# Optimization experiments

Measured on AMD Instinct MI355X. Metric: run time of the kernel, lower is better.

The kernel has to match this reference:

```python
import jax, jax.numpy as jnp
import numpy as np

jax.config.update("jax_enable_x64", True)

P = 2013265921        # NTT-friendly prime (15 * 2^27 + 1), stand-in for BLS12-381 Fr
G_ROOT = 31           # primitive root of P
LOG_N = 21
N = 1 << LOG_N


def _bit_reverse_perm(n):
    logn = n.bit_length() - 1
    idx = np.arange(n, dtype=np.int64)
    rev = np.zeros(n, dtype=np.int64)
    for b in range(logn):
        rev = (rev << 1) | ((idx >> b) & 1)
    return rev


def _pow_arr(base, exps, mod):
    # vectorized modular exponentiation over numpy int64 exponents (host-side, trace-time)
    res = np.ones_like(exps)
    b = np.int64(base % mod)
    e = exps.copy()
    while e.max() > 0:
        res = np.where(e & 1, (res * b) % mod, res)
        b = (b * b) % mod
        e >>= 1
    return res


_REV = _bit_reverse_perm(N)


def intt(x):
    """Inverse NTT over Z_P, radix-2 DIT with bit-reversal. x: [N] int64 in [0,P)."""
    root = pow(G_ROOT, (P - 1) // N, P)
    iroot = pow(root, P - 2, P)
    x = x[_REV]
    length = 2
    while length <= N:
        half = length // 2
        wlen = pow(iroot, N // length, P)
        tw = jnp.asarray(_pow_arr(wlen, np.arange(half, dtype=np.int64), P))  # [half]
        x = x.reshape(-1, length)
        even, odd = x[:, :half], x[:, half:]
        t = (odd * tw) % P                       # products < 2^62, exact in int64
        x = jnp.concatenate([(even + t) % P, (even - t) % P], axis=1).reshape(-1)
        length *= 2
    n_inv = pow(N, P - 2, P)
    return (x * n_inv) % P


def compress4(a, b, c, d, z):
    """zkp.compress: a + z*b + z^2*c + z^3*d  (mod P). z is a Python int challenge."""
    z1 = z % P
    z2 = (z1 * z1) % P
    z3 = (z2 * z1) % P
    return (a + (b * z1) % P + (c * z2) % P + (d * z3) % P) % P


def commit(poly, bases):
    """KZG commitment proxy: MSM reduced to a scalar-weighted sum of SRS bases."""
    scal = poly.astype(jnp.float32) * np.float32(1.0 / P)  # normalize field elems
    return jnp.einsum('n,nc->c', scal, bases)              # [3]


def reference(w_l, w_r, w_o, w_4, table1, table2, table3, table4,
              q_lookup, powers_of_g, zeta):
    # Round 1: wire polynomials via INTT + commitments via MSM
    w_l_poly = intt(w_l)
    w_r_poly = intt(w_r)
    w_o_poly = intt(w_o)
    w_4_poly = intt(w_4)

    # Lookup: compress tables with zeta, build query table f, split sorted multiset
    t_comp = compress4(table1, table2, table3, table4, zeta)
    table_poly = intt(t_comp)
    w_comp = compress4(w_l, w_r, w_o, w_4, zeta)
    f_comp = jnp.where(q_lookup != 0, w_comp, t_comp)      # compute_query_table
    f_poly = intt(f_comp)

    s = jnp.sort(jnp.concatenate([t_comp, f_comp]))        # combine_split
    h_1, h_2 = s[0::2], s[1::2]
    h_1_poly = intt(h_1)
    h_2_poly = intt(h_2)

    polys = jnp.stack([w_l_poly, w_r_poly, w_o_poly, w_4_poly,
                       table_poly, f_poly, h_1_poly, h_2_poly])  # [8, N]
    commits = jnp.stack([commit(p, powers_of_g) for p in polys])  # [8, 3]
    return commits, polys


def setup_inputs() -> dict:
    key = jax.random.key(0)
    ks = jax.random.split(key, 11)
    fe = lambda k: jax.random.randint(k, (N,), 0, P, dtype=jnp.int64)
    return {
        'w_l': fe(ks[0]), 'w_r': fe(ks[1]), 'w_o': fe(ks[2]), 'w_4': fe(ks[3]),
        'table1': fe(ks[4]), 'table2': fe(ks[5]), 'table3': fe(ks[6]), 'table4': fe(ks[7]),
        'q_lookup': jax.random.randint(ks[8], (N,), 0, 2, dtype=jnp.int64),
        'powers_of_g': jax.random.normal(ks[9], (N, 3), dtype=jnp.float32),
        'zeta': 987654321,
    }
```

## Files before the change

### kernel.cpp

```cpp
#include <hip/hip_runtime.h>
#include <stdint.h>

#define PRIME 2013265921u
#define LOGN 21
#define NN (1u << LOGN)

constexpr uint32_t cpow(uint64_t b, uint64_t e) {
    uint64_t r = 1;
    b %= PRIME;
    while (e) {
        if (e & 1ull) r = r * b % PRIME;
        b = b * b % PRIME;
        e >>= 1;
    }
    return (uint32_t)r;
}
constexpr uint32_t cpinv() {
    uint32_t inv = 1;
    for (int i = 0; i < 6; i++) inv *= 2u - PRIME * inv;
    return inv;
}
constexpr uint32_t NPRIME   = (uint32_t)(0u - cpinv());
constexpr uint32_t RMODP    = (uint32_t)((1ull << 32) % PRIME);
constexpr uint32_t ROOT     = cpow(31u, (PRIME - 1) / NN);
constexpr uint32_t IROOT    = cpow(ROOT, PRIME - 2);
constexpr uint32_t IROOT1K  = cpow(IROOT, 1024);
constexpr uint32_t NINV     = cpow(NN, PRIME - 2);
constexpr uint32_t NINV_M   = (uint32_t)((((uint64_t)NINV) << 32) % PRIME);

__device__ __forceinline__ uint32_t addmod(uint32_t a, uint32_t b) {
    uint32_t s = a + b; return (s >= PRIME) ? s - PRIME : s;
}
__device__ __forceinline__ uint32_t submod(uint32_t a, uint32_t b) {
    return (a >= b) ? (a - b) : (a + PRIME - b);
}
__device__ __forceinline__ uint32_t mulmod(uint32_t a, uint32_t b) {
    return (uint32_t)(((uint64_t)a * (uint64_t)b) % PRIME);
}
__device__ __forceinline__ uint32_t montmul(uint32_t a, uint32_t b) {
    uint64_t t = (uint64_t)a * b;
    uint32_t m = (uint32_t)t * NPRIME;
    uint32_t u = (uint32_t)((t + (uint64_t)m * PRIME) >> 32);
    return (u >= PRIME) ? u - PRIME : u;
}
__device__ uint32_t powmod(uint32_t b, uint32_t e) {
    uint32_t r = 1u;
    while (e) {
        if (e & 1u) r = mulmod(r, b);
        b = mulmod(b, b);
        e >>= 1;
    }
    return r;
}
__device__ __forceinline__ uint32_t tomont(uint32_t x) {
    return (uint32_t)((((uint64_t)x) << 32) % PRIME);
}

__global__ void twiddle_ab_kernel(uint32_t* __restrict__ A, uint32_t* __restrict__ B) {
    uint32_t i = blockIdx.x * blockDim.x + threadIdx.x;
    B[i] = tomont(powmod(IROOT, i));
    A[i] = tomont(powmod(IROOT1K, i));
}
__global__ void twiddle_compact_kernel(const uint32_t* __restrict__ A, const uint32_t* __restrict__ B,
                                       uint32_t* __restrict__ WT1, uint32_t* __restrict__ ROWT,
                                       uint32_t* __restrict__ CW) {
    uint32_t i = blockIdx.x * blockDim.x + threadIdx.x;
    if (i < 4096) {
        if (i == 0) WT1[0] = RMODP;
        else {
            uint32_t s = 31u - __clz(i);
            uint32_t j = i ^ (1u << s);
            uint32_t e = j << (20u - s);
            WT1[i] = montmul(A[e >> 10], B[e & 1023u]);
        }
    }
    if (i < 512) {
        if (i == 0) ROWT[0] = RMODP;
        else {
            uint32_t t = 31u - __clz(i);
            uint32_t e = (i - (1u << t)) << (20u - t);
            ROWT[i] = montmul(A[e >> 10], B[e & 1023u]);
        }
    }
    if (i < 36864) {
        uint32_t s = i >> 12, j = i & 4095u;
        uint32_t e = j << (8u - s);
        CW[i] = montmul(A[e >> 10], B[e & 1023u]);
    }
}

__global__ __launch_bounds__(256) void compress_kernel(
        const int* __restrict__ wl, const int* __restrict__ wr,
        const int* __restrict__ wo, const int* __restrict__ w4,
        const int* __restrict__ t1, const int* __restrict__ t2,
        const int* __restrict__ t3, const int* __restrict__ t4,
        const int* __restrict__ q,  const int* __restrict__ zp,
        uint32_t* __restrict__ tcomp, uint32_t* __restrict__ fcomp,
        unsigned int* __restrict__ hist64) {
    __shared__ unsigned int h64[64];
    if (threadIdx.x < 64) h64[threadIdx.x] = 0;
    __syncthreads();
    uint32_t z1 = ((uint32_t)zp[0]) % PRIME;
    uint32_t z2 = mulmod(z1, z1);
    uint32_t z3 = mulmod(z2, z1);
    for (uint32_t i = blockIdx.x * blockDim.x + threadIdx.x; i < NN; i += gridDim.x * blockDim.x) {
        uint32_t t = addmod(addmod((uint32_t)t1[i], mulmod((uint32_t)t2[i], z1)),
                            addmod(mulmod((uint32_t)t3[i], z2), mulmod((uint32_t)t4[i], z3)));
        uint32_t w = addmod(addmod((uint32_t)wl[i], mulmod((uint32_t)wr[i], z1)),
                            addmod(mulmod((uint32_t)wo[i], z2), mulmod((uint32_t)w4[i], z3)));
        uint32_t f = (q[i] != 0) ? w : t;
        tcomp[i] = t;
        fcomp[i] = f;
        atomicAdd(&h64[t >> 25], 1u);
        atomicAdd(&h64[f >> 25], 1u);
    }
    __syncthreads();
    if (threadIdx.x < 64 && h64[threadIdx.x])
        atomicAdd(&hist64[threadIdx.x], h64[threadIdx.x]);
}

#define NBUCK 8192

__global__ void scan64_kernel(const unsigned int* __restrict__ hist64,
                              unsigned int* __restrict__ cbase, unsigned int* __restrict__ ccursor) {
    if (threadIdx.x == 0) {
        unsigned int run = 0;
        for (int b = 0; b < 64; b++) { cbase[b] = run; ccursor[b] = run; run += hist64[b]; }
        cbase[64] = run;
    }
}

__global__ __launch_bounds__(256) void pass1_kernel(const uint32_t* __restrict__ tcomp,
                                                    const uint32_t* __restrict__ fcomp,
                                                    unsigned int* __restrict__ ccursor,
                                                    uint32_t* __restrict__ barr1) {
    __shared__ uint32_t grp[4096];
    __shared__ unsigned char grpb[4096];
    __shared__ unsigned int cnt[64], pref[64], curs[64], rbase[64];
    uint32_t base = blockIdx.x * 4096;
    uint32_t tid = threadIdx.x;
    if (tid < 64) cnt[tid] = 0;
    __syncthreads();
    for (uint32_t l = tid; l < 4096; l += 256) {
        uint32_t gi = base + l;
        uint32_t v = (gi < NN) ? tcomp[gi] : fcomp[gi - NN];
        atomicAdd(&cnt[v >> 25], 1u);
    }
    __syncthreads();
    if (tid == 0) {
        unsigned int run = 0;
        for (int b = 0; b < 64; b++) { pref[b] = run; curs[b] = run; run += cnt[b]; }
    }
    __syncthreads();
    if (tid < 64 && cnt[tid]) rbase[tid] = atomicAdd(&ccursor[tid], cnt[tid]);
    for (uint32_t l = tid; l < 4096; l += 256) {
        uint32_t gi = base + l;
        uint32_t v = (gi < NN) ? tcomp[gi] : fcomp[gi - NN];
        uint32_t b = v >> 25;
        unsigned int p = atomicAdd(&curs[b], 1u);
        grp[p] = v; grpb[p] = (unsigned char)b;
    }
    __syncthreads();
    for (uint32_t l = tid; l < 4096; l += 256) {
        uint32_t b = grpb[l];
        barr1[rbase[b] + (l - pref[b])] = grp[l];
    }
}

__global__ __launch_bounds__(256) void fine_hist_kernel(const uint32_t* __restrict__ barr1,
                                                        const unsigned int* __restrict__ cbase,
                                                        unsigned int* __restrict__ hist) {
    __shared__ unsigned int cnt[128];
    uint32_t tid = threadIdx.x;
    uint32_t reg = blockIdx.y;
    if (tid < 128) cnt[tid] = 0;
    __syncthreads();
    uint32_t lo = cbase[reg], hi = cbase[reg + 1];
    for (uint32_t i = lo + blockIdx.x * 256 + tid; i < hi; i += gridDim.x * 256)
        atomicAdd(&cnt[(barr1[i] >> 18) & 127u], 1u);
    __syncthreads();
    if (tid < 128 && cnt[tid]) atomicAdd(&hist[reg * 128 + tid], cnt[tid]);
}

__global__ void scan_kernel(const unsigned int* __restrict__ hist,
                            unsigned int* __restrict__ basearr, unsigned int* __restrict__ fcursor) {
    __shared__ unsigned int ls[256];
    int t = threadIdx.x;
    unsigned int local[32];
    unsigned int s = 0;
    for (int k = 0; k < 32; k++) { local[k] = hist[t * 32 + k]; s += local[k]; }
    ls[t] = s;
    __syncthreads();
    for (int off = 1; off < 256; off <<= 1) {
        unsigned int v = (t >= off) ? ls[t - off] : 0u;
        __syncthreads();
        ls[t] += v;
        __syncthreads();
    }
    unsigned int run = ls[t] - s;
    for (int k = 0; k < 32; k++) {
        basearr[t * 32 + k] = run;
        fcursor[t * 32 + k] = run;
        run += local[k];
    }
    if (t == 255) basearr[NBUCK] = run;
}

__global__ __launch_bounds__(256) void pass2_kernel(const uint32_t* __restrict__ barr1,
                                                    const unsigned int* __restrict__ cbase,
                                                    unsigned int* __restrict__ fcursor,
                                                    uint32_t* __restrict__ barr2) {
    __shared__ uint32_t grp[4096];
    __shared__ unsigned char grpb[4096];
    __shared__ unsigned int cnt[128], pref[128], curs[128], rbase[128];
    uint32_t tid = threadIdx.x;
    uint32_t reg = blockIdx.y;
    uint32_t lo = cbase[reg], hi = cbase[reg + 1];
    for (uint32_t start = lo + blockIdx.x * 4096; start < hi; start += gridDim.x * 4096) {
        uint32_t n = min(4096u, hi - start);
        if (tid < 128) cnt[tid] = 0;
        __syncthreads();
        for (uint32_t l = tid; l < n; l += 256)
            atomicAdd(&cnt[(barr1[start + l] >> 18) & 127u], 1u);
        __syncthreads();
        if (tid == 0) {
            unsigned int run = 0;
            for (int b = 0; b < 128; b++) { pref[b] = run; curs[b] = run; run += cnt[b]; }
        }
        __syncthreads();
        if (tid < 128 && cnt[tid]) rbase[tid] = atomicAdd(&fcursor[reg * 128 + tid], cnt[tid]);
        for (uint32_t l = tid; l < n; l += 256) {
            uint32_t v = barr1[start + l];
            uint32_t b = (v >> 18) & 127u;
            unsigned int p = atomicAdd(&curs[b], 1u);
            grp[p] = v; grpb[p] = (unsigned char)b;
        }
        __syncthreads();
        for (uint32_t l = tid; l < n; l += 256) {
            uint32_t b = grpb[l];
            barr2[rbase[b] + (l - pref[b])] = grp[l];
        }
        __syncthreads();
    }
}

__global__ __launch_bounds__(256) void bucket_sort_kernel(const uint32_t* __restrict__ barr,
                                                          const unsigned int* __restrict__ basearr,
                                                          uint32_t* __restrict__ h1, uint32_t* __restrict__ h2) {
    __shared__ uint32_t ord[4096];
    __shared__ unsigned int cnt[128], pref[128], curs[128];
    uint32_t b  = blockIdx.x;
    uint32_t lo = basearr[b], hi = basearr[b + 1];
    uint32_t n  = hi - lo;
    if (n == 0) return;
    if (n > 4096) n = 4096;
    uint32_t tid = threadIdx.x;
    if (tid < 128) cnt[tid] = 0;
    __syncthreads();
    for (uint32_t i = tid; i < n; i += 256)
        atomicAdd(&cnt[(barr[lo + i] >> 11) & 127u], 1u);
    __syncthreads();
    if (tid == 0) {
        unsigned int run = 0;
        for (int d = 0; d < 128; d++) { pref[d] = run; curs[d] = run; run += cnt[d]; }
    }
    __syncthreads();
    for (uint32_t i = tid; i < n; i += 256) {
        uint32_t v = barr[lo + i];
        uint32_t d = (v >> 11) & 127u;
        unsigned int p = atomicAdd(&curs[d], 1u);
        ord[p] = v;
    }
    __syncthreads();
    for (uint32_t p = tid; p < n; p += 256) {
        uint32_t v = ord[p];
        uint32_t d = (v >> 11) & 127u;
        uint32_t l0 = pref[d], l1 = l0 + cnt[d];
        uint32_t r = 0;
        for (uint32_t q = l0; q < l1; q++) {
            uint32_t u = ord[q];
            r += (u < v) || (u == v && q < p);
        }
        uint32_t gp = lo + l0 + r;
        if (gp & 1) h2[gp >> 1] = v; else h1[gp >> 1] = v;
    }
}

struct SrcPtrs { const uint32_t* p[8]; };

__global__ void bitrev_kernel(SrcPtrs srcs, uint32_t* __restrict__ dst) {
    __shared__ uint32_t tile[64 * 65];
    uint32_t poly = blockIdx.y;
    const uint32_t* src = srcs.p[poly];
    uint32_t* out = dst + (size_t)poly * NN;
    uint32_t m  = blockIdx.x;
    uint32_t rm = __brev(m) >> 23;
    for (uint32_t l = threadIdx.x; l < 4096; l += blockDim.x) {
        uint32_t u = l >> 6, v = l & 63;
        tile[u * 65 + v] = src[(u << 15) | (rm << 6) | v];
    }
    __syncthreads();
    for (uint32_t l = threadIdx.x; l < 4096; l += blockDim.x) {
        uint32_t a = l >> 6, b = l & 63;
        uint32_t ra = __brev(a) >> 26, rb = __brev(b) >> 26;
        out[(a << 15) | (m << 6) | b] = tile[rb * 65 + ra];
    }
}

__device__ __forceinline__ uint32_t padi(uint32_t i) { return i + (i >> 5); }

__global__ __launch_bounds__(256) void ntt_phase1_kernel(uint32_t* __restrict__ polys,
                                                         const uint32_t* __restrict__ WT1) {
    __shared__ uint32_t wt[4096];
    __shared__ uint32_t sd[4224];
    uint32_t* x = polys + (size_t)blockIdx.y * NN + (size_t)blockIdx.x * 4096;
    #pragma unroll
    for (uint32_t m = 0; m < 4; m++) {
        uint32_t l = m * 1024 + threadIdx.x * 4;
        uint4 v = *reinterpret_cast<const uint4*>(&x[l]);
        uint4 w = *reinterpret_cast<const uint4*>(&WT1[l]);
        uint32_t p = padi(l);
        sd[p] = v.x; sd[p + 1] = v.y; sd[p + 2] = v.z; sd[p + 3] = v.w;
        *reinterpret_cast<uint4*>(&wt[l]) = w;
    }
    __syncthreads();
    #pragma unroll
    for (int t = 0; t < 6; t++) {
        uint32_t h = 1u << (2 * t);
        #pragma unroll
        for (uint32_t m = 0; m < 4; m++) {
            uint32_t q = threadIdx.x + (m << 8);
            uint32_t j = q & (h - 1);
            uint32_t grp = q >> (2 * t);
            uint32_t i0 = (grp << (2 * t + 2)) + j;
            uint32_t w1  = wt[h + j];
            uint32_t w2  = wt[2 * h + j];
            uint32_t w2j = wt[3 * h + j];
            uint32_t p0 = padi(i0), p1 = padi(i0 + h), p2 = padi(i0 + 2 * h), p3 = padi(i0 + 3 * h);
            uint32_t a0 = sd[p0], a1 = sd[p1], a2 = sd[p2], a3 = sd[p3];
            uint32_t t1 = montmul(w1, a1), t3 = montmul(w1, a3);
            uint32_t b0 = addmod(a0, t1), b1 = submod(a0, t1);
            uint32_t b2 = addmod(a2, t3), b3 = submod(a2, t3);
            uint32_t u2 = montmul(w2, b2), u3 = montmul(w2j, b3);
            sd[p0] = addmod(b0, u2);
            sd[p2] = submod(b0, u2);
            sd[p1] = addmod(b1, u3);
            sd[p3] = submod(b1, u3);
        }
        __syncthreads();
    }
    #pragma unroll
    for (uint32_t m = 0; m < 4; m++) {
        uint32_t l = m * 1024 + threadIdx.x * 4;
        uint32_t p = padi(l);
        uint4 v;
        v.x = montmul(sd[p], NINV_M);
        v.y = montmul(sd[p + 1], NINV_M);
        v.z = montmul(sd[p + 2], NINV_M);
        v.w = montmul(sd[p + 3], NINV_M);
        *reinterpret_cast<uint4*>(&x[l]) = v;
    }
}

__global__ __launch_bounds__(512) void ntt_phase2_kernel(uint32_t* __restrict__ polys,
                                                         const uint32_t* __restrict__ ROWT,
                                                         const uint32_t* __restrict__ CW,
                                                         const float* __restrict__ g,
                                                         double* __restrict__ partials) {
    __shared__ __align__(16) uint32_t sd[16384];
    uint32_t b = blockIdx.x;
    uint32_t xcd = b & 7u, k = b >> 3;
    uint32_t poly = k >> 4;
    uint32_t c0_idx = xcd * 16u + (k & 15u);
    uint32_t* x = polys + (size_t)poly * NN;
    uint32_t c0 = c0_idx * 32u;
    uint32_t tid = threadIdx.x;
    uint32_t c = tid & 31u;
    uint32_t rt = tid >> 5;
    uint32_t cg = tid & 7u;
    uint32_t r0 = tid >> 3;

    #pragma unroll
    for (uint32_t kk = 0; kk < 8; kk++) {
        uint32_t row = r0 + kk * 64;
        uint4 v = *reinterpret_cast<const uint4*>(&x[(row << 12) + c0 + 4 * cg]);
        *reinterpret_cast<uint4*>(&sd[row * 32 + 4 * cg]) = v;
    }
    uint32_t cw[9];
    #pragma unroll
    for (int s = 0; s < 9; s++) cw[s] = CW[s * 4096 + c0 + c];
    __syncthreads();

    #pragma unroll
    for (int s = 0; s < 8; s += 2) {
        uint32_t h = 1u << s;
        #pragma unroll
        for (uint32_t m = 0; m < 8; m++) {
            uint32_t u = (rt << 3) + m;
            uint32_t kk = u & (h - 1);
            uint32_t grp = u >> s;
            uint32_t r = (grp << (s + 2)) + kk;
            uint32_t w1  = montmul(ROWT[h + kk], cw[s]);
            uint32_t w2  = montmul(ROWT[2 * h + kk], cw[s + 1]);
            uint32_t w2j = montmul(ROWT[3 * h + kk], cw[s + 1]);
            uint32_t i0 = (r << 5) + c;
            uint32_t i1 = ((r + h) << 5) + c;
            uint32_t i2 = ((r + 2 * h) << 5) + c;
            uint32_t i3 = ((r + 3 * h) << 5) + c;
            uint32_t a0 = sd[i0], a1 = sd[i1], a2 = sd[i2], a3 = sd[i3];
            uint32_t t1 = montmul(w1, a1), t3 = montmul(w1, a3);
            uint32_t b0 = addmod(a0, t1), b1 = submod(a0, t1);
            uint32_t b2 = addmod(a2, t3), b3 = submod(a2, t3);
            uint32_t u2 = montmul(w2, b2), u3 = montmul(w2j, b3);
            sd[i0] = addmod(b0, u2);
            sd[i2] = submod(b0, u2);
            sd[i1] = addmod(b1, u3);
            sd[i3] = submod(b1, u3);
        }
        __syncthreads();
    }
    #pragma unroll
    for (uint32_t m = 0; m < 16; m++) {
        uint32_t kk = (rt << 4) + m;
        uint32_t w = montmul(ROWT[256 + kk], cw[8]);
        uint32_t i0 = (kk << 5) + c, i1 = ((kk + 256) << 5) + c;
        uint32_t u = sd[i0];
        uint32_t v = montmul(sd[i1], w);
        sd[i0] = addmod(u, v);
        sd[i1] = submod(u, v);
    }
    __syncthreads();

    float* xf = (float*)x;
    const float invp = (float)(1.0 / 2013265921.0);
    double a0 = 0.0, a1 = 0.0, a2 = 0.0;
    #pragma unroll
    for (uint32_t kk = 0; kk < 8; kk++) {
        uint32_t row = r0 + kk * 64;
        uint32_t idx0 = (row << 12) + c0 + 4 * cg;
        uint32_t base = row * 32 + 4 * cg;
        float f0 = (float)sd[base], f1 = (float)sd[base + 1];
        float f2 = (float)sd[base + 2], f3 = (float)sd[base + 3];
        float4 fv = make_float4(f0, f1, f2, f3);
        *reinterpret_cast<float4*>(&xf[idx0]) = fv;
        const float4* gp = reinterpret_cast<const float4*>(&g[(size_t)idx0 * 3]);
        float4 g0 = gp[0], g1 = gp[1], g2 = gp[2];
        float s0 = f0 * invp, s1 = f1 * invp, s2 = f2 * invp, s3 = f3 * invp;
        a0 += (double)(s0 * g0.x) + (double)(s1 * g0.w) + (double)(s2 * g1.z) + (double)(s3 * g2.y);
        a1 += (double)(s0 * g0.y) + (double)(s1 * g1.x) + (double)(s2 * g1.w) + (double)(s3 * g2.z);
        a2 += (double)(s0 * g0.z) + (double)(s1 * g1.y) + (double)(s2 * g2.x) + (double)(s3 * g2.w);
    }
    __syncthreads();
    double* red = (double*)sd;
    double v3[3] = {a0, a1, a2};
    #pragma unroll
    for (int kq = 0; kq < 3; kq++) {
        red[tid] = v3[kq];
        __syncthreads();
        for (int off = 256; off > 0; off >>= 1) {
            if (tid < off) red[tid] += red[tid + off];
            __syncthreads();
        }
        if (tid == 0) partials[((size_t)poly * 128 + c0_idx) * 3 + kq] = red[0];
        __syncthreads();
    }
}

__global__ void reduce_commits_kernel(const double* __restrict__ partials, float* __restrict__ outf) {
    __shared__ double red[256];
    int t = threadIdx.x;
    for (int k = 0; k < 24; k++) {
        int p = k / 3, cc = k % 3;
        red[t] = (t < 128) ? partials[((size_t)p * 128 + t) * 3 + cc] : 0.0;
        __syncthreads();
        for (int off = 128; off > 0; off >>= 1) {
            if (t < off) red[t] += red[t + off];
            __syncthreads();
        }
        if (t == 0) outf[k] = (float)red[0];
        __syncthreads();
    }
}

extern "C" void kernel_launch(void* const* d_in, const int* in_sizes, int n_in,
                              void* d_out, int out_size, void* d_ws, size_t ws_size,
                              hipStream_t stream) {
    const int* wl = (const int*)d_in[0];
    const int* wr = (const int*)d_in[1];
    const int* wo = (const int*)d_in[2];
    const int* w4 = (const int*)d_in[3];
    const int* t1 = (const int*)d_in[4];
    const int* t2 = (const int*)d_in[5];
    const int* t3 = (const int*)d_in[6];
    const int* t4 = (const int*)d_in[7];
    const int* q  = (const int*)d_in[8];
    const float* g = (const float*)d_in[9];
    const int* zp = (const int*)d_in[10];

    char* ws = (char*)d_ws;
    uint32_t* WT1  = (uint32_t*)(ws);
    uint32_t* ROWT = (uint32_t*)(ws + (64u  << 10));
    uint32_t* CW   = (uint32_t*)(ws + (128u << 10));
    uint32_t* tcomp  = (uint32_t*)(ws + (8ull  << 20));
    uint32_t* fcomp  = (uint32_t*)(ws + (16ull << 20));
    uint32_t* h1     = (uint32_t*)(ws + (24ull << 20));
    uint32_t* h2     = (uint32_t*)(ws + (32ull << 20));
    unsigned int* hist    = (unsigned int*)(ws + (40ull << 20));
    unsigned int* basearr = (unsigned int*)(ws + (40ull << 20) + (64u  << 10));
    unsigned int* fcursor = (unsigned int*)(ws + (40ull << 20) + (128u << 10));
    uint32_t*     tA      = (uint32_t*)   (ws + (40ull << 20) + (200u << 10));
    uint32_t*     tB      = (uint32_t*)   (ws + (40ull << 20) + (208u << 10));
    unsigned int* hist64  = (unsigned int*)(ws + (40ull << 20) + (216u << 10));
    unsigned int* cbase   = (unsigned int*)(ws + (40ull << 20) + (224u << 10));
    unsigned int* ccursor = (unsigned int*)(ws + (40ull << 20) + (232u << 10));
    double*       partials = (double*)    (ws + (40ull << 20) + (256u << 10));

    float* outf = (float*)d_out;
    uint32_t* outpolys = (uint32_t*)outf + 24;
    uint32_t* barr1 = (uint32_t*)outf + 1024;
    uint32_t* barr2 = (uint32_t*)outf + 1024 + (5u << 20);

    hipMemsetAsync(hist, 0, NBUCK * sizeof(unsigned int), stream);
    hipMemsetAsync(hist64, 0, 64 * sizeof(unsigned int), stream);

    twiddle_ab_kernel<<<4, 256, 0, stream>>>(tA, tB);
    twiddle_compact_kernel<<<144, 256, 0, stream>>>(tA, tB, WT1, ROWT, CW);

    compress_kernel<<<2048, 256, 0, stream>>>(wl, wr, wo, w4, t1, t2, t3, t4, q, zp,
                                              tcomp, fcomp, hist64);
    scan64_kernel<<<1, 64, 0, stream>>>(hist64, cbase, ccursor);
    pass1_kernel<<<1024, 256, 0, stream>>>(tcomp, fcomp, ccursor, barr1);
    fine_hist_kernel<<<dim3(16, 64), 256, 0, stream>>>(barr1, cbase, hist);
    scan_kernel<<<1, 256, 0, stream>>>(hist, basearr, fcursor);
    pass2_kernel<<<dim3(16, 64), 256, 0, stream>>>(barr1, cbase, fcursor, barr2);
    bucket_sort_kernel<<<NBUCK, 256, 0, stream>>>(barr2, basearr, h1, h2);

    SrcPtrs sp;
    sp.p[0] = (const uint32_t*)wl;
    sp.p[1] = (const uint32_t*)wr;
    sp.p[2] = (const uint32_t*)wo;
    sp.p[3] = (const uint32_t*)w4;
    sp.p[4] = tcomp;
    sp.p[5] = fcomp;
    sp.p[6] = h1;
    sp.p[7] = h2;
    bitrev_kernel<<<dim3(512, 8), 256, 0, stream>>>(sp, outpolys);
    ntt_phase1_kernel<<<dim3(512, 8), 256, 0, stream>>>(outpolys, WT1);
    ntt_phase2_kernel<<<1024, 512, 0, stream>>>(outpolys, ROWT, CW, g, partials);

    reduce_commits_kernel<<<1, 256, 0, stream>>>(partials, outf);
}
```

Before: 322.3 us.

## Vectorize compress/pass1/bitrev loads, widen bucket digit, remap blocks across XCDs

The compress, pass1 and bitrev kernels now use 128-bit vector loads and stores with one fixed chunk per thread instead of grid-stride scalar loops, which cuts memory instruction count. The bucket sort's final digit grows from 128 to 256 sub-buckets, shortening the quadratic rank-counting scans. Bitrev and NTT phase1 switch to a 1D grid whose block index is remapped so each XCD handles a contiguous range of chunks, aiming for better L2 locality between the two kernels. The compress kernel now assumes exactly 2048 blocks of 256 threads cover N with 4 elements per thread.

```diff
diff --git a/kernel.cpp b/kernel.cpp
--- a/kernel.cpp
+++ b/kernel.cpp
@@ -103,17 +103,51 @@
     uint32_t z1 = ((uint32_t)zp[0]) % PRIME;
     uint32_t z2 = mulmod(z1, z1);
     uint32_t z3 = mulmod(z2, z1);
-    for (uint32_t i = blockIdx.x * blockDim.x + threadIdx.x; i < NN; i += gridDim.x * blockDim.x) {
-        uint32_t t = addmod(addmod((uint32_t)t1[i], mulmod((uint32_t)t2[i], z1)),
-                            addmod(mulmod((uint32_t)t3[i], z2), mulmod((uint32_t)t4[i], z3)));
-        uint32_t w = addmod(addmod((uint32_t)wl[i], mulmod((uint32_t)wr[i], z1)),
-                            addmod(mulmod((uint32_t)wo[i], z2), mulmod((uint32_t)w4[i], z3)));
-        uint32_t f = (q[i] != 0) ? w : t;
-        tcomp[i] = t;
-        fcomp[i] = f;
-        atomicAdd(&h64[t >> 25], 1u);
-        atomicAdd(&h64[f >> 25], 1u);
-    }
+    uint32_t i0 = (blockIdx.x * 256u + threadIdx.x) * 4u;
+    int4 a1 = *reinterpret_cast<const int4*>(&t1[i0]);
+    int4 a2 = *reinterpret_cast<const int4*>(&t2[i0]);
+    int4 a3 = *reinterpret_cast<const int4*>(&t3[i0]);
+    int4 a4 = *reinterpret_cast<const int4*>(&t4[i0]);
+    int4 b1 = *reinterpret_cast<const int4*>(&wl[i0]);
+    int4 b2 = *reinterpret_cast<const int4*>(&wr[i0]);
+    int4 b3 = *reinterpret_cast<const int4*>(&wo[i0]);
+    int4 b4 = *reinterpret_cast<const int4*>(&w4[i0]);
+    int4 qq = *reinterpret_cast<const int4*>(&q[i0]);
+    uint4 tv, fv;
+    {
+        uint32_t t = addmod(addmod((uint32_t)a1.x, mulmod((uint32_t)a2.x, z1)),
+                            addmod(mulmod((uint32_t)a3.x, z2), mulmod((uint32_t)a4.x, z3)));
+        uint32_t w = addmod(addmod((uint32_t)b1.x, mulmod((uint32_t)b2.x, z1)),
+                            addmod(mulmod((uint32_t)b3.x, z2), mulmod((uint32_t)b4.x, z3)));
+        tv.x = t; fv.x = (qq.x != 0) ? w : t;
+    }
+    {
+        uint32_t t = addmod(addmod((uint32_t)a1.y, mulmod((uint32_t)a2.y, z1)),
+                            addmod(mulmod((uint32_t)a3.y, z2), mulmod((uint32_t)a4.y, z3)));
+        uint32_t w = addmod(addmod((uint32_t)b1.y, mulmod((uint32_t)b2.y, z1)),
+                            addmod(mulmod((uint32_t)b3.y, z2), mulmod((uint32_t)b4.y, z3)));
+        tv.y = t; fv.y = (qq.y != 0) ? w : t;
+    }
+    {
+        uint32_t t = addmod(addmod((uint32_t)a1.z, mulmod((uint32_t)a2.z, z1)),
+                            addmod(mulmod((uint32_t)a3.z, z2), mulmod((uint32_t)a4.z, z3)));
+        uint32_t w = addmod(addmod((uint32_t)b1.z, mulmod((uint32_t)b2.z, z1)),
+                            addmod(mulmod((uint32_t)b3.z, z2), mulmod((uint32_t)b4.z, z3)));
+        tv.z = t; fv.z = (qq.z != 0) ? w : t;
+    }
+    {
+        uint32_t t = addmod(addmod((uint32_t)a1.w, mulmod((uint32_t)a2.w, z1)),
+                            addmod(mulmod((uint32_t)a3.w, z2), mulmod((uint32_t)a4.w, z3)));
+        uint32_t w = addmod(addmod((uint32_t)b1.w, mulmod((uint32_t)b2.w, z1)),
+                            addmod(mulmod((uint32_t)b3.w, z2), mulmod((uint32_t)b4.w, z3)));
+        tv.w = t; fv.w = (qq.w != 0) ? w : t;
+    }
+    *reinterpret_cast<uint4*>(&tcomp[i0]) = tv;
+    *reinterpret_cast<uint4*>(&fcomp[i0]) = fv;
+    atomicAdd(&h64[tv.x >> 25], 1u); atomicAdd(&h64[fv.x >> 25], 1u);
+    atomicAdd(&h64[tv.y >> 25], 1u); atomicAdd(&h64[fv.y >> 25], 1u);
+    atomicAdd(&h64[tv.z >> 25], 1u); atomicAdd(&h64[fv.z >> 25], 1u);
+    atomicAdd(&h64[tv.w >> 25], 1u); atomicAdd(&h64[fv.w >> 25], 1u);
     __syncthreads();
     if (threadIdx.x < 64 && h64[threadIdx.x])
         atomicAdd(&hist64[threadIdx.x], h64[threadIdx.x]);
@@ -137,14 +171,20 @@
     __shared__ uint32_t grp[4096];
     __shared__ unsigned char grpb[4096];
     __shared__ unsigned int cnt[64], pref[64], curs[64], rbase[64];
-    uint32_t base = blockIdx.x * 4096;
     uint32_t tid = threadIdx.x;
+    const uint32_t* srcp = (blockIdx.x < 512) ? (tcomp + blockIdx.x * 4096)
+                                              : (fcomp + (blockIdx.x - 512) * 4096);
     if (tid < 64) cnt[tid] = 0;
     __syncthreads();
-    for (uint32_t l = tid; l < 4096; l += 256) {
-        uint32_t gi = base + l;
-        uint32_t v = (gi < NN) ? tcomp[gi] : fcomp[gi - NN];
-        atomicAdd(&cnt[v >> 25], 1u);
+    uint4 vv[4];
+    #pragma unroll
+    for (uint32_t m = 0; m < 4; m++) {
+        uint32_t l = (m * 256u + tid) * 4u;
+        vv[m] = *reinterpret_cast<const uint4*>(&srcp[l]);
+        atomicAdd(&cnt[vv[m].x >> 25], 1u);
+        atomicAdd(&cnt[vv[m].y >> 25], 1u);
+        atomicAdd(&cnt[vv[m].z >> 25], 1u);
+        atomicAdd(&cnt[vv[m].w >> 25], 1u);
     }
     __syncthreads();
     if (tid == 0) {
@@ -153,12 +193,16 @@
     }
     __syncthreads();
     if (tid < 64 && cnt[tid]) rbase[tid] = atomicAdd(&ccursor[tid], cnt[tid]);
-    for (uint32_t l = tid; l < 4096; l += 256) {
-        uint32_t gi = base + l;
-        uint32_t v = (gi < NN) ? tcomp[gi] : fcomp[gi - NN];
-        uint32_t b = v >> 25;
-        unsigned int p = atomicAdd(&curs[b], 1u);
-        grp[p] = v; grpb[p] = (unsigned char)b;
+    #pragma unroll
+    for (uint32_t m = 0; m < 4; m++) {
+        uint32_t vs[4] = {vv[m].x, vv[m].y, vv[m].z, vv[m].w};
+        #pragma unroll
+        for (int j = 0; j < 4; j++) {
+            uint32_t v = vs[j];
+            uint32_t b = v >> 25;
+            unsigned int p = atomicAdd(&curs[b], 1u);
+            grp[p] = v; grpb[p] = (unsigned char)b;
+        }
     }
     __syncthreads();
     for (uint32_t l = tid; l < 4096; l += 256) {
@@ -248,38 +292,38 @@
                                                           const unsigned int* __restrict__ basearr,
                                                           uint32_t* __restrict__ h1, uint32_t* __restrict__ h2) {
     __shared__ uint32_t ord[4096];
-    __shared__ unsigned int cnt[128], pref[128], curs[128];
+    __shared__ unsigned int cnt[256], pref[256], curs[256];
     uint32_t b  = blockIdx.x;
     uint32_t lo = basearr[b], hi = basearr[b + 1];
     uint32_t n  = hi - lo;
     if (n == 0) return;
     if (n > 4096) n = 4096;
     uint32_t tid = threadIdx.x;
-    if (tid < 128) cnt[tid] = 0;
+    cnt[tid] = 0;
     __syncthreads();
     for (uint32_t i = tid; i < n; i += 256)
-        atomicAdd(&cnt[(barr[lo + i] >> 11) & 127u], 1u);
+        atomicAdd(&cnt[(barr[lo + i] >> 10) & 255u], 1u);
     __syncthreads();
     if (tid == 0) {
         unsigned int run = 0;
-        for (int d = 0; d < 128; d++) { pref[d] = run; curs[d] = run; run += cnt[d]; }
+        for (int d = 0; d < 256; d++) { pref[d] = run; curs[d] = run; run += cnt[d]; }
     }
     __syncthreads();
     for (uint32_t i = tid; i < n; i += 256) {
         uint32_t v = barr[lo + i];
-        uint32_t d = (v >> 11) & 127u;
+        uint32_t d = (v >> 10) & 255u;
         unsigned int p = atomicAdd(&curs[d], 1u);
         ord[p] = v;
     }
     __syncthreads();
     for (uint32_t p = tid; p < n; p += 256) {
         uint32_t v = ord[p];
-        uint32_t d = (v >> 11) & 127u;
+        uint32_t d = (v >> 10) & 255u;
         uint32_t l0 = pref[d], l1 = l0 + cnt[d];
         uint32_t r = 0;
-        for (uint32_t q = l0; q < l1; q++) {
-            uint32_t u = ord[q];
-            r += (u < v) || (u == v && q < p);
+        for (uint32_t qq = l0; qq < l1; qq++) {
+            uint32_t u = ord[qq];
+            r += (u < v) || (u == v && qq < p);
         }
         uint32_t gp = lo + l0 + r;
         if (gp & 1) h2[gp >> 1] = v; else h1[gp >> 1] = v;
@@ -288,22 +332,36 @@
 
 struct SrcPtrs { const uint32_t* p[8]; };
 
-__global__ void bitrev_kernel(SrcPtrs srcs, uint32_t* __restrict__ dst) {
+__global__ __launch_bounds__(256) void bitrev_kernel(SrcPtrs srcs, uint32_t* __restrict__ dst) {
     __shared__ uint32_t tile[64 * 65];
-    uint32_t poly = blockIdx.y;
+    uint32_t bb = blockIdx.x;
+    uint32_t xcd = bb & 7u, k = bb >> 3;
+    uint32_t poly = k >> 6;
+    uint32_t m = (k & 63u) + xcd * 64u;
     const uint32_t* src = srcs.p[poly];
     uint32_t* out = dst + (size_t)poly * NN;
-    uint32_t m  = blockIdx.x;
     uint32_t rm = __brev(m) >> 23;
-    for (uint32_t l = threadIdx.x; l < 4096; l += blockDim.x) {
-        uint32_t u = l >> 6, v = l & 63;
-        tile[u * 65 + v] = src[(u << 15) | (rm << 6) | v];
-    }
-    __syncthreads();
-    for (uint32_t l = threadIdx.x; l < 4096; l += blockDim.x) {
-        uint32_t a = l >> 6, b = l & 63;
-        uint32_t ra = __brev(a) >> 26, rb = __brev(b) >> 26;
-        out[(a << 15) | (m << 6) | b] = tile[rb * 65 + ra];
+    uint32_t tid = threadIdx.x;
+    #pragma unroll
+    for (uint32_t mm = 0; mm < 4; mm++) {
+        uint32_t l = (mm * 256u + tid) * 4u;
+        uint32_t u = l >> 6, v = l & 63u;
+        uint4 x = *reinterpret_cast<const uint4*>(&src[(u << 15) | (rm << 6) | v]);
+        uint32_t base = u * 65u + v;
+        tile[base] = x.x; tile[base + 1] = x.y; tile[base + 2] = x.z; tile[base + 3] = x.w;
+    }
+    __syncthreads();
+    #pragma unroll
+    for (uint32_t mm = 0; mm < 4; mm++) {
+        uint32_t l = (mm * 256u + tid) * 4u;
+        uint32_t a = l >> 6, b4 = l & 63u;
+        uint32_t ra = __brev(a) >> 26;
+        uint4 x;
+        x.x = tile[(__brev(b4)     >> 26) * 65u + ra];
+        x.y = tile[(__brev(b4 + 1) >> 26) * 65u + ra];
+        x.z = tile[(__brev(b4 + 2) >> 26) * 65u + ra];
+        x.w = tile[(__brev(b4 + 3) >> 26) * 65u + ra];
+        *reinterpret_cast<uint4*>(&out[(a << 15) | (m << 6) | b4]) = x;
     }
 }
 
@@ -313,7 +371,11 @@
                                                          const uint32_t* __restrict__ WT1) {
     __shared__ uint32_t wt[4096];
     __shared__ uint32_t sd[4224];
-    uint32_t* x = polys + (size_t)blockIdx.y * NN + (size_t)blockIdx.x * 4096;
+    uint32_t bb = blockIdx.x;
+    uint32_t xcd = bb & 7u, k = bb >> 3;
+    uint32_t poly = k >> 6;
+    uint32_t chunk = (k & 63u) + xcd * 64u;
+    uint32_t* x = polys + (size_t)poly * NN + (size_t)chunk * 4096;
     #pragma unroll
     for (uint32_t m = 0; m < 4; m++) {
         uint32_t l = m * 1024 + threadIdx.x * 4;
@@ -544,8 +606,8 @@
     sp.p[5] = fcomp;
     sp.p[6] = h1;
     sp.p[7] = h2;
-    bitrev_kernel<<<dim3(512, 8), 256, 0, stream>>>(sp, outpolys);
-    ntt_phase1_kernel<<<dim3(512, 8), 256, 0, stream>>>(outpolys, WT1);
+    bitrev_kernel<<<4096, 256, 0, stream>>>(sp, outpolys);
+    ntt_phase1_kernel<<<4096, 256, 0, stream>>>(outpolys, WT1);
     ntt_phase2_kernel<<<1024, 512, 0, stream>>>(outpolys, ROWT, CW, g, partials);
 
     reduce_commits_kernel<<<1, 256, 0, stream>>>(partials, outf);
```

Result: no change. 326.8 us (+1.4%).
